# Kernel optimization log

Measured on AMD Instinct MI355X. Metric: run time of the kernel, lower is better.

The kernel has to match this reference:

```python
import jax, jax.numpy as jnp
import numpy as np

C = 128   # channel_num
S = 56    # spatial size
K = 3     # ksize -> gaussian kernel is 2K x 2K = 6x6


def _gaussian_bank(theta, p, sig, a):
    # Vectorized version of get_gaussian over all (i, u) channel pairs.
    coords = jnp.linspace(-K, K, 2 * K)
    xv, yv = jnp.meshgrid(coords, coords, indexing='ij')  # [2K, 2K]
    ct = jnp.cos(theta)[:, :, None, None]                  # [C, C, 1, 1]
    st = jnp.sin(theta)[:, :, None, None]
    xrot = xv * ct + yv * st                               # [C, C, 2K, 2K]
    yrot = -xv * st + yv * ct
    p2 = (p ** 2)[:, :, None, None]
    s2 = (sig ** 2)[:, :, None, None]
    amp = (a / (2.0 * jnp.pi * p * sig))[:, :, None, None]
    return amp * jnp.exp(-0.5 * (xrot ** 2 / p2 + yrot ** 2 / s2))  # [C, C, 2K, 2K]


def setup_inputs() -> dict:
    key = jax.random.key(0)
    ks = jax.random.split(key, 8)
    scale = 90.0
    theta = scale * jnp.abs(jax.random.normal(ks[0], (C, C)))
    p = scale * jnp.abs(jax.random.normal(ks[1], (C, C))) + 10.0
    sig = scale * jnp.abs(jax.random.normal(ks[2], (C, C))) + 10.0
    a = scale * jnp.abs(jax.random.normal(ks[3], (C, C)))
    nI = jnp.abs(jax.random.normal(ks[4], (C, C)))
    nU = jnp.abs(jax.random.normal(ks[5], (C,)))
    bias = jnp.abs(jax.random.normal(ks[6], (C,)))
    # positive activations (module assumes post-ReLU input; pow of negatives -> NaN)
    x = jax.random.uniform(ks[7], (2, C, S, S), dtype=jnp.float32)
    return {"x": x, "theta": theta, "p": p, "sig": sig, "a": a,
            "nI": nI, "nU": nU, "bias": bias}


def reference(x, theta, p, sig, a, nI, nU, bias):
    B = x.shape[0]
    g = _gaussian_bank(theta, p, sig, a)                     # [C, C, 2K, 2K]
    # x[b,i]^nI[i,u] for all pairs -> [B, C, C, S, S]
    xp = x[:, :, None, :, :] ** nI[None, :, :, None, None]
    xp = xp.reshape(B, C * C, S, S)
    kern = g.reshape(C * C, 1, 2 * K, 2 * K)
    # depthwise cross-correlation per (i,u) pair; even kernel + pad K -> S+1,
    # then crop first row/col (matches output[1:, 1:] in the torch code)
    conv = jax.lax.conv_general_dilated(
        xp, kern, window_strides=(1, 1), padding=((K, K), (K, K)),
        feature_group_count=C * C)                           # [B, C*C, S+1, S+1]
    conv = conv[:, :, 1:, 1:].reshape(B, C, C, S, S)
    denom = (bias ** nU)[None, :, None, None] + conv.sum(axis=2)  # [B, C, S, S]
    num = x ** nU[None, :, None, None]
    return num / denom
```

## Files before the change

### kernel.cpp

```cpp
#include <hip/hip_runtime.h>
#include <math.h>

#define CN 128
#define SN 56
#define PCOLS 33
#define PXS 660
#define SDW 330
#define DYS (6 * PXS + PCOLS)
#define DXS (PXS + 1)
#define LOG2E 1.44269504088896341f

typedef float    fr4 __attribute__((ext_vector_type(4)));
typedef _Float16 hf8 __attribute__((ext_vector_type(8)));
typedef __fp16   pkv __attribute__((ext_vector_type(2)));

__device__ __forceinline__ int h2i(pkv h) {
    union { pkv h; int i; } u; u.h = h; return u.i;
}

__global__ void bank_kernel(const float* __restrict__ theta,
                            const float* __restrict__ p,
                            const float* __restrict__ sig,
                            const float* __restrict__ a,
                            unsigned short* __restrict__ bank) {
    int t = blockIdx.x * 256 + threadIdx.x;
    int lane = t & 63;
    int grp  = t >> 6;
    int nt = grp % 3;
    int ks = (grp / 3) & 3;
    int c  = grp / 12;
    int tap = nt * 16 + (lane & 15);
    int ub  = ks * 32 + (lane >> 4) * 8;
    hf8 v = {0,0,0,0,0,0,0,0};
    if (tap < 36) {
        int ky = tap / 6, kx = tap - ky * 6;
        float xv = -3.0f + 1.2f * ky;
        float yv = -3.0f + 1.2f * kx;
        #pragma unroll
        for (int j = 0; j < 8; ++j) {
            int pr = c * CN + ub + j;
            float th = theta[pr], pv = p[pr], sv = sig[pr], av = a[pr];
            float ct = __cosf(th), st = __sinf(th);
            float xr =  xv * ct + yv * st;
            float yr = -xv * st + yv * ct;
            float e  = -0.5f * (xr * xr / (pv * pv) + yr * yr / (sv * sv));
            float g  = (av / (2.0f * 3.14159265358979323846f * pv * sv))
                       * __builtin_amdgcn_exp2f(e * LOG2E);
            v[j] = (_Float16)g;
        }
    }
    ((hf8*)bank)[t] = v;
}

__global__ __launch_bounds__(512, 4) void divnorm_mfma(
        const float* __restrict__ x, const unsigned short* __restrict__ bank,
        const float* __restrict__ nI, const float* __restrict__ nU,
        const float* __restrict__ bias, float* __restrict__ out)
{
    __shared__ alignas(16) unsigned short SH[36 * PXS];
    int* SD = (int*)SH;

    const int bid = blockIdx.x;
    const int w   = bid & 1;
    const int h   = (bid >> 1) & 1;
    const int c   = (bid >> 2) & 127;
    const int b   = bid >> 9;
    const int tid = threadIdx.x;
    const int lane = tid & 63;
    const int wv   = tid >> 6;
    const int l15  = lane & 15;
    const int lg   = lane >> 4;

    hf8 Bf[3][4];
    {
        const hf8* bp = (const hf8*)bank + (size_t)c * 768 + lane;
        #pragma unroll
        for (int ks = 0; ks < 4; ++ks)
            #pragma unroll
            for (int nt = 0; nt < 3; ++nt)
                Bf[nt][ks] = bp[(ks * 3 + nt) * 64];
    }

    float nIr[4][8];
    {
        const float* nc = nI + c * CN;
        #pragma unroll
        for (int ks = 0; ks < 4; ++ks) {
            const float4* q = (const float4*)(nc + ks * 32 + lg * 8);
            float4 q0 = q[0], q1 = q[1];
            nIr[ks][0] = q0.x; nIr[ks][1] = q0.y; nIr[ks][2] = q0.z; nIr[ks][3] = q0.w;
            nIr[ks][4] = q1.x; nIr[ks][5] = q1.y; nIr[ks][6] = q1.z; nIr[ks][7] = q1.w;
        }
    }

    const float* xc = x   + (size_t)(b * CN + c) * (SN * SN);
    float*       oc = out + (size_t)(b * CN + c) * (SN * SN);
    const float nUc = nU[c];
    const float bn  = __builtin_amdgcn_exp2f(nUc * __builtin_amdgcn_logf(bias[c]));
    const int   c0m2 = 28 * w - 2;

    const int pof0 = l15 * SDW;
    const int pof1 = (16 + l15) * SDW;
    const int pof2 = (32 + l15) * SDW;

    #pragma unroll 1
    for (int phase = 0; phase < 2; ++phase) {
        const int r0   = 28 * h + 14 * phase;
        const int r0m2 = r0 - 2;
        const int tb   = phase ? 10 : 0;
        const int nit  = phase ? ((wv < 6) ? 4 : 3) : 5;

        int pidx = (tb + wv) * 16 + l15;
        int prl  = pidx / PCOLS;
        int pcl  = pidx - prl * PCOLS;
        int prow = r0m2 + prl;
        int pcol = c0m2 + pcl;
        bool val = ((unsigned)prow < 56u) && ((unsigned)pcol < 56u);
        float xv = xc[val ? (prow * SN + pcol) : 0];

        #pragma unroll 1
        for (int i = 0; i < nit; ++i) {
            float L = val ? __builtin_amdgcn_logf(xv) : -1e30f;

            {
                int np   = pidx + 128;
                int nprl = np / PCOLS;
                int npcl = np - nprl * PCOLS;
                int nprw = r0m2 + nprl;
                int npcc = c0m2 + npcl;
                val = ((unsigned)nprw < 56u) && ((unsigned)npcc < 56u);
                xv  = xc[val ? (nprw * SN + npcc) : 0];
                pidx = np;
            }

            fr4 a0 = {0.f,0.f,0.f,0.f}, a1 = {0.f,0.f,0.f,0.f}, a2 = {0.f,0.f,0.f,0.f};
            #pragma unroll
            for (int ks = 0; ks < 4; ++ks) {
                float t[8];
                #pragma unroll
                for (int j = 0; j < 8; ++j)
                    t[j] = __builtin_amdgcn_exp2f(nIr[ks][j] * L);
                union { pkv h[4]; hf8 v; } af;
                af.h[0] = __builtin_amdgcn_cvt_pkrtz(t[0], t[1]);
                af.h[1] = __builtin_amdgcn_cvt_pkrtz(t[2], t[3]);
                af.h[2] = __builtin_amdgcn_cvt_pkrtz(t[4], t[5]);
                af.h[3] = __builtin_amdgcn_cvt_pkrtz(t[6], t[7]);
                a0 = __builtin_amdgcn_mfma_f32_16x16x32_f16(af.v, Bf[0][ks], a0, 0, 0, 0);
                a1 = __builtin_amdgcn_mfma_f32_16x16x32_f16(af.v, Bf[1][ks], a1, 0, 0, 0);
                a2 = __builtin_amdgcn_mfma_f32_16x16x32_f16(af.v, Bf[2][ks], a2, 0, 0, 0);
            }

            int pbd = (tb + wv + 8 * i) * 8 + lg * 2;
            int2 v0, v1;
            v0.x = h2i(__builtin_amdgcn_cvt_pkrtz(a0[0], a0[1]));
            v0.y = h2i(__builtin_amdgcn_cvt_pkrtz(a0[2], a0[3]));
            v1.x = h2i(__builtin_amdgcn_cvt_pkrtz(a1[0], a1[1]));
            v1.y = h2i(__builtin_amdgcn_cvt_pkrtz(a1[2], a1[3]));
            *(int2*)&SD[pof0 + pbd] = v0;
            *(int2*)&SD[pof1 + pbd] = v1;
            if (l15 < 4) {
                int2 v2;
                v2.x = h2i(__builtin_amdgcn_cvt_pkrtz(a2[0], a2[1]));
                v2.y = h2i(__builtin_amdgcn_cvt_pkrtz(a2[2], a2[3]));
                *(int2*)&SD[pof2 + pbd] = v2;
            }
        }
        __syncthreads();

        if (tid < 14 * 28) {
            int oy = tid / 28;
            int ox = tid - oy * 28;
            const unsigned short* pb = &SH[oy * PCOLS + ox];
            float s = 0.0f;
            #pragma unroll
            for (int dy = 0; dy < 6; ++dy)
                #pragma unroll
                for (int dx = 0; dx < 6; ++dx)
                    s += (float)(*(const _Float16*)&pb[dy * DYS + dx * DXS]);
            int y  = r0 + oy;
            int xg = c0m2 + 2 + ox;
            float xq  = xc[y * SN + xg];
            float num = __builtin_amdgcn_exp2f(nUc * __builtin_amdgcn_logf(xq));
            oc[y * SN + xg] = num / (bn + s);
        }
        __syncthreads();

        if (phase == 0) {
            for (int idx = tid; idx < 36 * 80; idx += 512) {
                int pl  = idx / 80;
                int off = idx - pl * 80;
                SD[pl * SDW + off] = SD[pl * SDW + 231 + off];
            }
            __syncthreads();
        }
    }
}

extern "C" void kernel_launch(void* const* d_in, const int* in_sizes, int n_in,
                              void* d_out, int out_size, void* d_ws, size_t ws_size,
                              hipStream_t stream) {
    const float* x     = (const float*)d_in[0];
    const float* theta = (const float*)d_in[1];
    const float* p     = (const float*)d_in[2];
    const float* sig   = (const float*)d_in[3];
    const float* a     = (const float*)d_in[4];
    const float* nI    = (const float*)d_in[5];
    const float* nU    = (const float*)d_in[6];
    const float* bias  = (const float*)d_in[7];
    float* out = (float*)d_out;
    unsigned short* bank = (unsigned short*)d_ws;

    hipLaunchKernelGGL(bank_kernel, dim3(384), dim3(256), 0, stream,
                       theta, p, sig, a, bank);
    hipLaunchKernelGGL(divnorm_mfma, dim3(2 * CN * 4), dim3(512), 0, stream,
                       x, bank, nI, nU, bias, out);
}
```

Baseline: 101.8 us.

## Tile full-width 56-column rows with 4 row phases to cut halo recompute

Each block now covers a full-width half of the image, 28 rows by 56 columns, instead of a 28x28 quadrant. It processes 7-row phases over a 64-column padded tile and carries the 5-row halo between phases in shared memory. This removes the duplicated column-halo work (pow, exp and MFMA on overlapping pixels) between left and right blocks and halves the grid. In exchange it adds more phases and barriers per block, uses more shared memory (which may lower occupancy), and leaves fewer blocks to spread across the CUs.

After: 97.99 us. -3.7%, faster.

```diff
diff --git a/kernel.cpp b/kernel.cpp
--- a/kernel.cpp
+++ b/kernel.cpp
@@ -3,11 +3,10 @@
 
 #define CN 128
 #define SN 56
-#define PCOLS 33
-#define PXS 660
-#define SDW 330
-#define DYS (6 * PXS + PCOLS)
-#define DXS (PXS + 1)
+#define PXS 772
+#define SDW 386
+#define DYS 4696
+#define DXS 773
 #define LOG2E 1.44269504088896341f
 
 typedef float    fr4 __attribute__((ext_vector_type(4)));
@@ -58,13 +57,13 @@
         const float* __restrict__ bias, float* __restrict__ out)
 {
     __shared__ alignas(16) unsigned short SH[36 * PXS];
-    int* SD = (int*)SH;
+    int*  SD  = (int*)SH;
+    int2* SD2 = (int2*)SH;
 
     const int bid = blockIdx.x;
-    const int w   = bid & 1;
-    const int h   = (bid >> 1) & 1;
-    const int c   = (bid >> 2) & 127;
-    const int b   = bid >> 9;
+    const int h   = bid & 1;
+    const int c   = (bid >> 1) & 127;
+    const int b   = bid >> 8;
     const int tid = threadIdx.x;
     const int lane = tid & 63;
     const int wv   = tid >> 6;
@@ -97,37 +96,44 @@
     float*       oc = out + (size_t)(b * CN + c) * (SN * SN);
     const float nUc = nU[c];
     const float bn  = __builtin_amdgcn_exp2f(nUc * __builtin_amdgcn_logf(bias[c]));
-    const int   c0m2 = 28 * w - 2;
 
     const int pof0 = l15 * SDW;
     const int pof1 = (16 + l15) * SDW;
     const int pof2 = (32 + l15) * SDW;
 
+    const int oy = tid / 56;
+    const int ox = tid - oy * 56;
+
     #pragma unroll 1
-    for (int phase = 0; phase < 2; ++phase) {
-        const int r0   = 28 * h + 14 * phase;
+    for (int ph = 0; ph < 4; ++ph) {
+        const int r0   = 28 * h + 7 * ph;
         const int r0m2 = r0 - 2;
-        const int tb   = phase ? 10 : 0;
-        const int nit  = phase ? ((wv < 6) ? 4 : 3) : 5;
+        const int tb   = ph ? 20 : 0;
+
+        if (ph > 0) {
+            __syncthreads();
+            for (int idx = tid; idx < 36 * 80; idx += 512) {
+                int pl  = idx / 80;
+                int off = idx - pl * 80;
+                SD2[pl * 193 + off] = SD2[pl * 193 + 112 + off];
+            }
+            __syncthreads();
+        }
 
         int pidx = (tb + wv) * 16 + l15;
-        int prl  = pidx / PCOLS;
-        int pcl  = pidx - prl * PCOLS;
-        int prow = r0m2 + prl;
-        int pcol = c0m2 + pcl;
+        int prow = r0m2 + (pidx >> 6);
+        int pcol = (pidx & 63) - 2;
         bool val = ((unsigned)prow < 56u) && ((unsigned)pcol < 56u);
         float xv = xc[val ? (prow * SN + pcol) : 0];
 
         #pragma unroll 1
-        for (int i = 0; i < nit; ++i) {
+        for (int tile = tb + wv; tile < 48; tile += 8) {
             float L = val ? __builtin_amdgcn_logf(xv) : -1e30f;
 
             {
                 int np   = pidx + 128;
-                int nprl = np / PCOLS;
-                int npcl = np - nprl * PCOLS;
-                int nprw = r0m2 + nprl;
-                int npcc = c0m2 + npcl;
+                int nprw = r0m2 + (np >> 6);
+                int npcc = (np & 63) - 2;
                 val = ((unsigned)nprw < 56u) && ((unsigned)npcc < 56u);
                 xv  = xc[val ? (nprw * SN + npcc) : 0];
                 pidx = np;
@@ -150,7 +156,7 @@
                 a2 = __builtin_amdgcn_mfma_f32_16x16x32_f16(af.v, Bf[2][ks], a2, 0, 0, 0);
             }
 
-            int pbd = (tb + wv + 8 * i) * 8 + lg * 2;
+            int pbd = tile * 8 + lg * 2;
             int2 v0, v1;
             v0.x = h2i(__builtin_amdgcn_cvt_pkrtz(a0[0], a0[1]));
             v0.y = h2i(__builtin_amdgcn_cvt_pkrtz(a0[2], a0[3]));
@@ -167,31 +173,18 @@
         }
         __syncthreads();
 
-        if (tid < 14 * 28) {
-            int oy = tid / 28;
-            int ox = tid - oy * 28;
-            const unsigned short* pb = &SH[oy * PCOLS + ox];
+        if (tid < 7 * 56) {
+            const unsigned short* pb = &SH[oy * 64 + ox];
             float s = 0.0f;
             #pragma unroll
             for (int dy = 0; dy < 6; ++dy)
                 #pragma unroll
                 for (int dx = 0; dx < 6; ++dx)
                     s += (float)(*(const _Float16*)&pb[dy * DYS + dx * DXS]);
-            int y  = r0 + oy;
-            int xg = c0m2 + 2 + ox;
-            float xq  = xc[y * SN + xg];
+            int y = r0 + oy;
+            float xq  = xc[y * SN + ox];
             float num = __builtin_amdgcn_exp2f(nUc * __builtin_amdgcn_logf(xq));
-            oc[y * SN + xg] = num / (bn + s);
-        }
-        __syncthreads();
-
-        if (phase == 0) {
-            for (int idx = tid; idx < 36 * 80; idx += 512) {
-                int pl  = idx / 80;
-                int off = idx - pl * 80;
-                SD[pl * SDW + off] = SD[pl * SDW + 231 + off];
-            }
-            __syncthreads();
+            oc[y * SN + ox] = num / (bn + s);
         }
     }
 }
@@ -212,6 +205,6 @@
 
     hipLaunchKernelGGL(bank_kernel, dim3(384), dim3(256), 0, stream,
                        theta, p, sig, a, bank);
-    hipLaunchKernelGGL(divnorm_mfma, dim3(2 * CN * 4), dim3(512), 0, stream,
+    hipLaunchKernelGGL(divnorm_mfma, dim3(4 * CN), dim3(512), 0, stream,
                        x, bank, nI, nU, bias, out);
 }
```
